# Kernel tuning notes

Measured on AMD Instinct MI355X. Metric: run time of the kernel, lower is better.

## Reference

```python
import jax, jax.numpy as jnp
import numpy as np

NUM_HEADS = 8
NUM_GROUPS = 8
EPS = 1e-5


def group_norm(x, scale, bias):
    # x: [B, C, H, W]; GroupNorm with NUM_GROUPS groups, per-channel affine.
    B, C, H, W = x.shape
    xg = x.reshape(B, NUM_GROUPS, C // NUM_GROUPS, H, W)
    mean = jnp.mean(xg, axis=(2, 3, 4), keepdims=True)
    var = jnp.var(xg, axis=(2, 3, 4), keepdims=True)
    xg = (xg - mean) * jax.lax.rsqrt(var + EPS)
    xn = xg.reshape(B, C, H, W)
    return xn * scale[None, :, None, None] + bias[None, :, None, None]


def setup_inputs() -> dict:
    key = jax.random.key(0)
    ks = jax.random.split(key, 4)
    B, C, H, W = 8, 256, 32, 32
    x = jax.random.normal(ks[0], (B, C, H, W), dtype=jnp.float32)
    gn_scale = jnp.ones((C,), dtype=jnp.float32)
    gn_bias = jnp.zeros((C,), dtype=jnp.float32)
    w_qkv = jax.random.normal(ks[1], (3 * C, C), dtype=jnp.float32) * (1.0 / np.sqrt(C))
    b_qkv = jnp.zeros((3 * C,), dtype=jnp.float32)
    w_out = jax.random.normal(ks[2], (C, C), dtype=jnp.float32) * (1.0 / np.sqrt(C))
    b_out = jnp.zeros((C,), dtype=jnp.float32)
    return {"x": x, "gn_scale": gn_scale, "gn_bias": gn_bias,
            "w_qkv": w_qkv, "b_qkv": b_qkv, "w_out": w_out, "b_out": b_out}


def reference(x, gn_scale, gn_bias, w_qkv, b_qkv, w_out, b_out):
    B, C, H, W = x.shape
    hd = C // NUM_HEADS  # head_dim
    N = H * W

    h = group_norm(x, gn_scale, gn_bias)
    # 1x1 conv == channel matmul: [B, 3C, H, W]
    qkv = jnp.einsum('oc,bchw->bohw', w_qkv, h) + b_qkv[None, :, None, None]
    q, k, v = jnp.split(qkv, 3, axis=1)
    # [B, heads, head_dim, N]
    q = q.reshape(B, NUM_HEADS, hd, N)
    k = k.reshape(B, NUM_HEADS, hd, N)
    v = v.reshape(B, NUM_HEADS, hd, N)

    scale = 1.0 / np.sqrt(hd).astype(np.float32)
    attn = jnp.einsum('bhdn,bhdm->bhnm', q, k) * scale  # [B, h, N, N]
    attn = jax.nn.softmax(attn, axis=-1)
    out = jnp.einsum('bhnm,bhdm->bhdn', attn, v)  # [B, h, hd, N]
    out = out.reshape(B, C, H, W)
    out = jnp.einsum('oc,bchw->bohw', w_out, out) + b_out[None, :, None, None]
    return x + out
```

## Files before the change

### kernel.cpp

```cpp
#include <hip/hip_runtime.h>
#include <hip/hip_bf16.h>
#include <math.h>

#define BB 8
#define CC 256
#define NN 1024
#define HEADS 8
#define HDIM 32
#define NGRP 8

using bf16x8 = __attribute__((ext_vector_type(8))) short;
using f32x4  = __attribute__((ext_vector_type(4))) float;

#if __has_builtin(__builtin_amdgcn_exp2f)
#define EXP2(x) __builtin_amdgcn_exp2f(x)
#else
#define EXP2(x) exp2f(x)
#endif

#define SCL_Q_LOG2E 0.2550348892803828f

static __device__ __forceinline__ ushort f2bf(float x) {
  union { __hip_bfloat16 b; ushort u; } c;
  c.b = __float2bfloat16(x);
  return c.u;
}

__global__ __launch_bounds__(256) void wcast_kernel(
    const float* __restrict__ wqkv, const float* __restrict__ wout,
    ushort* __restrict__ wbf)
{
  const int gid = blockIdx.x * 256 + threadIdx.x;
  const int e8 = gid * 8;
  const float* src = (e8 < 196608) ? (wqkv + e8) : (wout + (e8 - 196608));
  const float4 a = *(const float4*)src;
  const float4 c = *(const float4*)(src + 4);
  union { uint4 v; ushort s[8]; } o;
  o.s[0] = f2bf(a.x); o.s[1] = f2bf(a.y); o.s[2] = f2bf(a.z); o.s[3] = f2bf(a.w);
  o.s[4] = f2bf(c.x); o.s[5] = f2bf(c.y); o.s[6] = f2bf(c.z); o.s[7] = f2bf(c.w);
  *(uint4*)(wbf + e8) = o.v;
}

__global__ __launch_bounds__(1024) void gn_kernel(
    const float* __restrict__ x, const float* __restrict__ gns,
    const float* __restrict__ gnb, ushort* __restrict__ h)
{
  const int t = threadIdx.x;
  const int b = blockIdx.x >> 3, g = blockIdx.x & 7;
  const size_t base = (((size_t)b * CC + (size_t)g * 32) * NN);
  const float4* x4 = (const float4*)(x + base);
  ushort* hb = h + base;

  float4 r[8];
  float s = 0.f, ss = 0.f;
#pragma unroll
  for (int j = 0; j < 8; ++j) {
    r[j] = x4[t + j * 1024];
    s  += r[j].x + r[j].y + r[j].z + r[j].w;
    ss += r[j].x * r[j].x + r[j].y * r[j].y + r[j].z * r[j].z + r[j].w * r[j].w;
  }
#pragma unroll
  for (int off = 32; off > 0; off >>= 1) {
    s  += __shfl_down(s, off);
    ss += __shfl_down(ss, off);
  }
  __shared__ float rs[16], rss[16];
  __shared__ float smean, srstd;
  const int wid = t >> 6, lane = t & 63;
  if (lane == 0) { rs[wid] = s; rss[wid] = ss; }
  __syncthreads();
  if (t == 0) {
    float S = 0.f, SS = 0.f;
    for (int i = 0; i < 16; ++i) { S += rs[i]; SS += rss[i]; }
    const float mean = S * (1.f / 32768.f);
    const float var = SS * (1.f / 32768.f) - mean * mean;
    smean = mean;
    srstd = rsqrtf(var + 1e-5f);
  }
  __syncthreads();
  const float mean = smean, rstd = srstd;
#pragma unroll
  for (int j = 0; j < 8; ++j) {
    const int c = g * 32 + (t >> 8) + 4 * j;
    const float sc = gns[c] * rstd;
    const float bi = gnb[c];
    ushort4 w4;
    w4.x = f2bf((r[j].x - mean) * sc + bi);
    w4.y = f2bf((r[j].y - mean) * sc + bi);
    w4.z = f2bf((r[j].z - mean) * sc + bi);
    w4.w = f2bf((r[j].w - mean) * sc + bi);
    *(ushort4*)&hb[(size_t)(t + j * 1024) * 4] = w4;
  }
}

__global__ __launch_bounds__(256) void transpose_kernel(
    const ushort* __restrict__ h, ushort* __restrict__ hT)
{
  __shared__ ushort Ls[64 * 68];
  const int t = threadIdx.x;
  const int b = blockIdx.z;
  const int c0 = blockIdx.y << 6, n0 = blockIdx.x << 6;
  const ushort* hb = h + ((size_t)b * CC) * NN;

#pragma unroll
  for (int li = 0; li < 2; ++li) {
    const int id = t + (li << 8);
    const int cR = id >> 3, nC = id & 7;
    union { uint4 v; ushort s[8]; } xv;
    xv.v = *(const uint4*)(hb + (size_t)(c0 + cR) * NN + n0 + nC * 8);
#pragma unroll
    for (int j = 0; j < 8; ++j) Ls[(nC * 8 + j) * 68 + cR] = xv.s[j];
  }
  __syncthreads();
#pragma unroll
  for (int li = 0; li < 2; ++li) {
    const int id = t + (li << 8);
    const int nR = id >> 3, cP = id & 7;
    union { uint4 v; ushort4 s[2]; } ov;
    ov.s[0] = *(const ushort4*)&Ls[nR * 68 + cP * 8];
    ov.s[1] = *(const ushort4*)&Ls[nR * 68 + cP * 8 + 4];
    *(uint4*)(hT + ((size_t)b * NN + n0 + nR) * CC + c0 + cP * 8) = ov.v;
  }
}

template <int MODE>
__global__ __launch_bounds__(256) void conv_mfma_kernel(
    const ushort* __restrict__ Wbf, const float* __restrict__ bias,
    const ushort* __restrict__ X, const float* __restrict__ xres,
    ushort* __restrict__ qT, ushort* __restrict__ kT, ushort* __restrict__ vN,
    float* __restrict__ out)
{
  const int t = threadIdx.x;
  const int w = t >> 6, l = t & 63;
  const int lg = l >> 4, lr = l & 15;
  const int wr = w >> 1, wc = w & 1;
  const int b = blockIdx.z;
  const int o0 = blockIdx.y << 6, n0 = blockIdx.x << 6;

  __shared__ ushort Ws[64][72];
  __shared__ ushort Xs[64][72];

  union FragU { ushort4 u[2]; bf16x8 f; };
  f32x4 acc[2][2] = {};

  const ushort* Xb = X + (size_t)b * 1024 * 256;

  for (int k0 = 0; k0 < 256; k0 += 64) {
    __syncthreads();
#pragma unroll
    for (int li = 0; li < 2; ++li) {
      const int id = t + (li << 8);
      const int rr = id >> 3, c8 = id & 7;
      const uint4 wv = *(const uint4*)(Wbf + (size_t)(o0 + rr) * 256 + k0 + c8 * 8);
      *(uint4*)&Ws[rr][c8 * 8] = wv;
      const uint4 xv = *(const uint4*)(Xb + (size_t)(n0 + rr) * 256 + k0 + c8 * 8);
      *(uint4*)&Xs[rr][c8 * 8] = xv;
    }
    __syncthreads();

    FragU af[2][2], xf[2][2];
#pragma unroll
    for (int i = 0; i < 2; ++i)
#pragma unroll
      for (int kc = 0; kc < 2; ++kc) {
        const ushort* p = &Ws[wr * 32 + i * 16 + lr][kc * 32 + lg * 4];
        af[i][kc].u[0] = *(const ushort4*)p;
        af[i][kc].u[1] = *(const ushort4*)(p + 16);
        const ushort* q = &Xs[wc * 32 + i * 16 + lr][kc * 32 + lg * 4];
        xf[i][kc].u[0] = *(const ushort4*)q;
        xf[i][kc].u[1] = *(const ushort4*)(q + 16);
      }
#pragma unroll
    for (int ms = 0; ms < 2; ++ms)
#pragma unroll
      for (int ns = 0; ns < 2; ++ns) {
        acc[ms][ns] = __builtin_amdgcn_mfma_f32_16x16x32_bf16(af[ms][0].f, xf[ns][0].f, acc[ms][ns], 0, 0, 0);
        acc[ms][ns] = __builtin_amdgcn_mfma_f32_16x16x32_bf16(af[ms][1].f, xf[ns][1].f, acc[ms][ns], 0, 0, 0);
      }
  }

  if (MODE == 0) {
    const int sec = o0 >> 8;
    const float scl = (sec == 0) ? SCL_Q_LOG2E : 1.0f;
#pragma unroll
    for (int ms = 0; ms < 2; ++ms) {
      const int ob = o0 + wr * 32 + ms * 16 + lg * 4;
      const float4 b4 = *(const float4*)(bias + ob);
      const int oo = ob & 255;
      const int hh = oo >> 5, d0 = oo & 31;
      const int bh = b * 8 + hh;
#pragma unroll
      for (int ns = 0; ns < 2; ++ns) {
        const int n = n0 + wc * 32 + ns * 16 + lr;
        float v0 = (acc[ms][ns][0] + b4.x) * scl;
        float v1 = (acc[ms][ns][1] + b4.y) * scl;
        float v2 = (acc[ms][ns][2] + b4.z) * scl;
        float v3 = (acc[ms][ns][3] + b4.w) * scl;
        if (sec < 2) {
          ushort* dst = (sec == 0) ? qT : kT;
          ushort4 w4 = {f2bf(v0), f2bf(v1), f2bf(v2), f2bf(v3)};
          *(ushort4*)&dst[((size_t)bh * 1024 + n) * 32 + d0] = w4;
        } else {
          vN[((size_t)bh * 32 + d0 + 0) * 1024 + n] = f2bf(v0);
          vN[((size_t)bh * 32 + d0 + 1) * 1024 + n] = f2bf(v1);
          vN[((size_t)bh * 32 + d0 + 2) * 1024 + n] = f2bf(v2);
          vN[((size_t)bh * 32 + d0 + 3) * 1024 + n] = f2bf(v3);
        }
      }
    }
  } else {
#pragma unroll
    for (int ms = 0; ms < 2; ++ms) {
      const int ob = o0 + wr * 32 + ms * 16 + lg * 4;
      const float4 b4 = *(const float4*)(bias + ob);
#pragma unroll
      for (int ns = 0; ns < 2; ++ns) {
        const int n = n0 + wc * 32 + ns * 16 + lr;
        const size_t i0 = ((size_t)b * 256 + ob) * 1024 + n;
        out[i0]          = acc[ms][ns][0] + b4.x + xres[i0];
        out[i0 + 1024]   = acc[ms][ns][1] + b4.y + xres[i0 + 1024];
        out[i0 + 2048]   = acc[ms][ns][2] + b4.z + xres[i0 + 2048];
        out[i0 + 3072]   = acc[ms][ns][3] + b4.w + xres[i0 + 3072];
      }
    }
  }
}

__global__ __launch_bounds__(256) void attn_kernel(
    const ushort* __restrict__ qT, const ushort* __restrict__ kT,
    const ushort* __restrict__ vN, ushort* __restrict__ aoT)
{
  const int t = threadIdx.x;
  const int w = t >> 6, l = t & 63;
  const int lg = l >> 4, lr = l & 15;
  const int bh = blockIdx.y;
  const int b = bh >> 3, hh = bh & 7;
  const int qbase = blockIdx.x << 6;

  __shared__ ushort Ks[128][40];
  __shared__ ushort Vs[32][136];

  union FragU { ushort4 u[2]; bf16x8 f; };

  FragU qf;
  {
    const ushort* Qp = qT + (((size_t)bh * 1024 + qbase + w * 16 + lr) * 32) + lg * 4;
    qf.u[0] = *(const ushort4*)Qp;
    qf.u[1] = *(const ushort4*)(Qp + 16);
  }

  f32x4 accO[2] = {};
  float m_st = -1e30f, l_st = 0.f;

  const ushort* Kbh = kT + (size_t)bh * 1024 * 32;
  const ushort* Vbh = vN + (size_t)bh * 32 * 1024;

  for (int m0 = 0; m0 < NN; m0 += 128) {
    __syncthreads();
    {
      const uint4* kp4 = (const uint4*)(Kbh + (size_t)m0 * 32);
      const uint4 kv0 = kp4[t], kv1 = kp4[t + 256];
      *(uint4*)&Ks[t >> 2][(t & 3) * 8] = kv0;
      *(uint4*)&Ks[64 + (t >> 2)][(t & 3) * 8] = kv1;
      const int d = t >> 4, m8 = (t & 15) * 8;
      const uint4 vv0 = *(const uint4*)(Vbh + (size_t)d * 1024 + m0 + m8);
      const uint4 vv1 = *(const uint4*)(Vbh + (size_t)(d + 16) * 1024 + m0 + m8);
      *(uint4*)&Vs[d][m8] = vv0;
      *(uint4*)&Vs[d + 16][m8] = vv1;
    }
    __syncthreads();

    f32x4 s[8];
#pragma unroll
    for (int ms = 0; ms < 8; ++ms) {
      FragU kf;
      const ushort* kp = &Ks[ms * 16 + lr][lg * 4];
      kf.u[0] = *(const ushort4*)kp;
      kf.u[1] = *(const ushort4*)(kp + 16);
      f32x4 z = {0.f, 0.f, 0.f, 0.f};
      s[ms] = __builtin_amdgcn_mfma_f32_16x16x32_bf16(kf.f, qf.f, z, 0, 0, 0);
    }

    float mx = s[0][0];
#pragma unroll
    for (int ms = 0; ms < 8; ++ms)
#pragma unroll
      for (int r = 0; r < 4; ++r) mx = fmaxf(mx, s[ms][r]);
    mx = fmaxf(mx, __shfl_xor(mx, 16));
    mx = fmaxf(mx, __shfl_xor(mx, 32));
    const float mnew = fmaxf(m_st, mx);
    const float c = EXP2(m_st - mnew);
    m_st = mnew;
    float ls = 0.f;
#pragma unroll
    for (int ms = 0; ms < 8; ++ms)
#pragma unroll
      for (int r = 0; r < 4; ++r) {
        const float p = EXP2(s[ms][r] - mnew);
        s[ms][r] = p;
        ls += p;
      }
    ls += __shfl_xor(ls, 16);
    ls += __shfl_xor(ls, 32);
    l_st = l_st * c + ls;
#pragma unroll
    for (int dt = 0; dt < 2; ++dt)
#pragma unroll
      for (int r = 0; r < 4; ++r) accO[dt][r] *= c;

    bf16x8 pb[4];
#pragma unroll
    for (int mc = 0; mc < 4; ++mc) {
      bf16x8 f;
#pragma unroll
      for (int r = 0; r < 4; ++r) {
        f[r]     = (short)f2bf(s[2 * mc][r]);
        f[r + 4] = (short)f2bf(s[2 * mc + 1][r]);
      }
      pb[mc] = f;
    }

#pragma unroll
    for (int dt = 0; dt < 2; ++dt) {
#pragma unroll
      for (int mc = 0; mc < 4; ++mc) {
        FragU vf;
        const ushort* vp = &Vs[dt * 16 + lr][mc * 32 + lg * 4];
        vf.u[0] = *(const ushort4*)vp;
        vf.u[1] = *(const ushort4*)(vp + 16);
        accO[dt] = __builtin_amdgcn_mfma_f32_16x16x32_bf16(vf.f, pb[mc], accO[dt], 0, 0, 0);
      }
    }
  }

  const float inv = 1.f / l_st;
  const int n = qbase + w * 16 + lr;
  ushort* ap = aoT + ((size_t)b * 1024 + n) * 256 + hh * 32 + lg * 4;
#pragma unroll
  for (int dt = 0; dt < 2; ++dt) {
    ushort4 w4;
    w4.x = f2bf(accO[dt][0] * inv);
    w4.y = f2bf(accO[dt][1] * inv);
    w4.z = f2bf(accO[dt][2] * inv);
    w4.w = f2bf(accO[dt][3] * inv);
    *(ushort4*)(ap + dt * 16) = w4;
  }
}

extern "C" void kernel_launch(void* const* d_in, const int* in_sizes, int n_in,
                              void* d_out, int out_size, void* d_ws, size_t ws_size,
                              hipStream_t stream)
{
  const float* x    = (const float*)d_in[0];
  const float* gns  = (const float*)d_in[1];
  const float* gnb  = (const float*)d_in[2];
  const float* wqkv = (const float*)d_in[3];
  const float* bqkv = (const float*)d_in[4];
  const float* wout = (const float*)d_in[5];
  const float* bout = (const float*)d_in[6];
  float* out = (float*)d_out;

  char* ws = (char*)d_ws;
  ushort* h   = (ushort*)(ws);
  ushort* hT  = (ushort*)(ws + (4u << 20));
  ushort* qT  = (ushort*)(ws + (8u << 20));
  ushort* kT  = (ushort*)(ws + (12u << 20));
  ushort* vN  = (ushort*)(ws + (16u << 20));
  ushort* aoT = (ushort*)(ws + (20u << 20));
  ushort* wbf = (ushort*)(ws + (24u << 20));

  wcast_kernel<<<dim3(128), dim3(256), 0, stream>>>(wqkv, wout, wbf);
  gn_kernel<<<dim3(64), dim3(1024), 0, stream>>>(x, gns, gnb, h);
  transpose_kernel<<<dim3(16, 4, 8), dim3(256), 0, stream>>>(h, hT);
  conv_mfma_kernel<0><<<dim3(16, 12, 8), dim3(256), 0, stream>>>(
      wbf, bqkv, hT, nullptr, qT, kT, vN, nullptr);
  attn_kernel<<<dim3(16, 64), dim3(256), 0, stream>>>(qT, kT, vN, aoT);
  conv_mfma_kernel<1><<<dim3(16, 4, 8), dim3(256), 0, stream>>>(
      wbf + 768 * 256, bout, aoT, x, nullptr, nullptr, nullptr, out);
}
```

Before: 127.7 us.

## Split GroupNorm into parallel partial stats, fuse normalize with transpose, prefetch K/V

GroupNorm statistics now come from 1024 small blocks whose partial sums a second tiny kernel reduces, replacing 64 large blocks that left most of the GPU idle. Normalization is folded into the transpose kernel, which reads fp32 x directly, so the intermediate bf16 h buffer and one kernel pass are gone. The attention kernel also prefetches the next K/V tile into registers while the current tile is computed. This adds one kernel launch and a second read of x, plus extra register pressure in attention.

```diff
diff --git a/kernel.cpp b/kernel.cpp
--- a/kernel.cpp
+++ b/kernel.cpp
@@ -41,75 +41,75 @@
   *(uint4*)(wbf + e8) = o.v;
 }
 
-__global__ __launch_bounds__(1024) void gn_kernel(
-    const float* __restrict__ x, const float* __restrict__ gns,
-    const float* __restrict__ gnb, ushort* __restrict__ h)
-{
-  const int t = threadIdx.x;
-  const int b = blockIdx.x >> 3, g = blockIdx.x & 7;
-  const size_t base = (((size_t)b * CC + (size_t)g * 32) * NN);
-  const float4* x4 = (const float4*)(x + base);
-  ushort* hb = h + base;
-
-  float4 r[8];
-  float s = 0.f, ss = 0.f;
-#pragma unroll
-  for (int j = 0; j < 8; ++j) {
-    r[j] = x4[t + j * 1024];
-    s  += r[j].x + r[j].y + r[j].z + r[j].w;
-    ss += r[j].x * r[j].x + r[j].y * r[j].y + r[j].z * r[j].z + r[j].w * r[j].w;
-  }
+__global__ __launch_bounds__(256) void gn_stats1(
+    const float* __restrict__ x, float2* __restrict__ part)
+{
+  const int p = blockIdx.x, t = threadIdx.x;
+  const float4* src = (const float4*)x + (size_t)p * 512;
+  const float4 a = src[t], b = src[t + 256];
+  float s  = a.x + a.y + a.z + a.w + b.x + b.y + b.z + b.w;
+  float ss = a.x*a.x + a.y*a.y + a.z*a.z + a.w*a.w
+           + b.x*b.x + b.y*b.y + b.z*b.z + b.w*b.w;
 #pragma unroll
   for (int off = 32; off > 0; off >>= 1) {
     s  += __shfl_down(s, off);
     ss += __shfl_down(ss, off);
   }
-  __shared__ float rs[16], rss[16];
-  __shared__ float smean, srstd;
+  __shared__ float rs[4], rss[4];
   const int wid = t >> 6, lane = t & 63;
   if (lane == 0) { rs[wid] = s; rss[wid] = ss; }
   __syncthreads();
   if (t == 0) {
-    float S = 0.f, SS = 0.f;
-    for (int i = 0; i < 16; ++i) { S += rs[i]; SS += rss[i]; }
-    const float mean = S * (1.f / 32768.f);
-    const float var = SS * (1.f / 32768.f) - mean * mean;
-    smean = mean;
-    srstd = rsqrtf(var + 1e-5f);
-  }
-  __syncthreads();
-  const float mean = smean, rstd = srstd;
-#pragma unroll
-  for (int j = 0; j < 8; ++j) {
-    const int c = g * 32 + (t >> 8) + 4 * j;
-    const float sc = gns[c] * rstd;
-    const float bi = gnb[c];
-    ushort4 w4;
-    w4.x = f2bf((r[j].x - mean) * sc + bi);
-    w4.y = f2bf((r[j].y - mean) * sc + bi);
-    w4.z = f2bf((r[j].z - mean) * sc + bi);
-    w4.w = f2bf((r[j].w - mean) * sc + bi);
-    *(ushort4*)&hb[(size_t)(t + j * 1024) * 4] = w4;
-  }
-}
-
-__global__ __launch_bounds__(256) void transpose_kernel(
-    const ushort* __restrict__ h, ushort* __restrict__ hT)
+    float2 o;
+    o.x = rs[0] + rs[1] + rs[2] + rs[3];
+    o.y = rss[0] + rss[1] + rss[2] + rss[3];
+    part[p] = o;
+  }
+}
+
+__global__ __launch_bounds__(64) void gn_stats2(
+    const float2* __restrict__ part, float2* __restrict__ stats)
+{
+  const int g = blockIdx.x, l = threadIdx.x;
+  float s = 0.f, ss = 0.f;
+  if (l < 16) { const float2 pp = part[g * 16 + l]; s = pp.x; ss = pp.y; }
+#pragma unroll
+  for (int off = 8; off > 0; off >>= 1) {
+    s  += __shfl_down(s, off);
+    ss += __shfl_down(ss, off);
+  }
+  if (l == 0) {
+    const float mean = s * (1.f / 32768.f);
+    const float var = ss * (1.f / 32768.f) - mean * mean;
+    float2 o; o.x = mean; o.y = rsqrtf(var + 1e-5f);
+    stats[g] = o;
+  }
+}
+
+__global__ __launch_bounds__(256) void gnt_kernel(
+    const float* __restrict__ x, const float2* __restrict__ stats,
+    const float* __restrict__ gns, const float* __restrict__ gnb,
+    ushort* __restrict__ hT)
 {
   __shared__ ushort Ls[64 * 68];
   const int t = threadIdx.x;
   const int b = blockIdx.z;
   const int c0 = blockIdx.y << 6, n0 = blockIdx.x << 6;
-  const ushort* hb = h + ((size_t)b * CC) * NN;
-
-#pragma unroll
-  for (int li = 0; li < 2; ++li) {
+
+#pragma unroll
+  for (int li = 0; li < 4; ++li) {
     const int id = t + (li << 8);
-    const int cR = id >> 3, nC = id & 7;
-    union { uint4 v; ushort s[8]; } xv;
-    xv.v = *(const uint4*)(hb + (size_t)(c0 + cR) * NN + n0 + nC * 8);
-#pragma unroll
-    for (int j = 0; j < 8; ++j) Ls[(nC * 8 + j) * 68 + cR] = xv.s[j];
+    const int row = id >> 4, col4 = id & 15;
+    const int c = c0 + row;
+    const float2 st = stats[b * 8 + (c >> 5)];
+    const float sc = gns[c] * st.y;
+    const float sh = gnb[c] - st.x * sc;
+    const float4 v = *(const float4*)(x + ((size_t)b * CC + c) * NN + n0 + col4 * 4);
+    const int nb = col4 * 4;
+    Ls[(nb + 0) * 68 + row] = f2bf(v.x * sc + sh);
+    Ls[(nb + 1) * 68 + row] = f2bf(v.y * sc + sh);
+    Ls[(nb + 2) * 68 + row] = f2bf(v.z * sc + sh);
+    Ls[(nb + 3) * 68 + row] = f2bf(v.w * sc + sh);
   }
   __syncthreads();
 #pragma unroll
@@ -254,21 +254,32 @@
 
   const ushort* Kbh = kT + (size_t)bh * 1024 * 32;
   const ushort* Vbh = vN + (size_t)bh * 32 * 1024;
+  const uint4* Kt = (const uint4*)Kbh;
+  const int vd = t >> 4, vm8 = (t & 15) * 8;
+
+  uint4 kr0, kr1, vr0, vr1;
+  {
+    kr0 = Kt[t];
+    kr1 = Kt[t + 256];
+    vr0 = *(const uint4*)(Vbh + (size_t)vd * 1024 + vm8);
+    vr1 = *(const uint4*)(Vbh + (size_t)(vd + 16) * 1024 + vm8);
+  }
 
   for (int m0 = 0; m0 < NN; m0 += 128) {
     __syncthreads();
-    {
-      const uint4* kp4 = (const uint4*)(Kbh + (size_t)m0 * 32);
-      const uint4 kv0 = kp4[t], kv1 = kp4[t + 256];
-      *(uint4*)&Ks[t >> 2][(t & 3) * 8] = kv0;
-      *(uint4*)&Ks[64 + (t >> 2)][(t & 3) * 8] = kv1;
-      const int d = t >> 4, m8 = (t & 15) * 8;
-      const uint4 vv0 = *(const uint4*)(Vbh + (size_t)d * 1024 + m0 + m8);
-      const uint4 vv1 = *(const uint4*)(Vbh + (size_t)(d + 16) * 1024 + m0 + m8);
-      *(uint4*)&Vs[d][m8] = vv0;
-      *(uint4*)&Vs[d + 16][m8] = vv1;
-    }
+    *(uint4*)&Ks[t >> 2][(t & 3) * 8] = kr0;
+    *(uint4*)&Ks[64 + (t >> 2)][(t & 3) * 8] = kr1;
+    *(uint4*)&Vs[vd][vm8] = vr0;
+    *(uint4*)&Vs[vd + 16][vm8] = vr1;
     __syncthreads();
+
+    if (m0 + 128 < NN) {
+      const int mn = m0 + 128;
+      kr0 = Kt[mn * 4 + t];
+      kr1 = Kt[mn * 4 + t + 256];
+      vr0 = *(const uint4*)(Vbh + (size_t)vd * 1024 + mn + vm8);
+      vr1 = *(const uint4*)(Vbh + (size_t)(vd + 16) * 1024 + mn + vm8);
+    }
 
     f32x4 s[8];
 #pragma unroll
@@ -361,17 +372,19 @@
   float* out = (float*)d_out;
 
   char* ws = (char*)d_ws;
-  ushort* h   = (ushort*)(ws);
-  ushort* hT  = (ushort*)(ws + (4u << 20));
-  ushort* qT  = (ushort*)(ws + (8u << 20));
-  ushort* kT  = (ushort*)(ws + (12u << 20));
-  ushort* vN  = (ushort*)(ws + (16u << 20));
-  ushort* aoT = (ushort*)(ws + (20u << 20));
-  ushort* wbf = (ushort*)(ws + (24u << 20));
+  ushort* hT    = (ushort*)(ws);
+  ushort* qT    = (ushort*)(ws + (4u << 20));
+  ushort* kT    = (ushort*)(ws + (8u << 20));
+  ushort* vN    = (ushort*)(ws + (12u << 20));
+  ushort* aoT   = (ushort*)(ws + (16u << 20));
+  ushort* wbf   = (ushort*)(ws + (20u << 20));
+  float2* part  = (float2*)(ws + (21u << 20));
+  float2* stats = (float2*)(ws + (21u << 20) + 8192);
 
   wcast_kernel<<<dim3(128), dim3(256), 0, stream>>>(wqkv, wout, wbf);
-  gn_kernel<<<dim3(64), dim3(1024), 0, stream>>>(x, gns, gnb, h);
-  transpose_kernel<<<dim3(16, 4, 8), dim3(256), 0, stream>>>(h, hT);
+  gn_stats1<<<dim3(1024), dim3(256), 0, stream>>>(x, part);
+  gn_stats2<<<dim3(64), dim3(64), 0, stream>>>(part, stats);
+  gnt_kernel<<<dim3(16, 4, 8), dim3(256), 0, stream>>>(x, stats, gns, gnb, hT);
   conv_mfma_kernel<0><<<dim3(16, 12, 8), dim3(256), 0, stream>>>(
       wbf, bqkv, hT, nullptr, qT, kT, vN, nullptr);
   attn_kernel<<<dim3(16, 64), dim3(256), 0, stream>>>(qT, kT, vN, aoT);
```

After: 128.1 us. About the same (+0.3%).
